# Optimization experiments

Measured on AMD Instinct MI355X. Metric: run time of the kernel, lower is better.

The kernel has to match this reference:

```python
import jax, jax.numpy as jnp
import numpy as np

DIM = 2048
N_HEADS = 16
HEAD_DIM = DIM // N_HEADS
ROPE_BASE = 10000.0


def rope_cos_sin(T, head_dim, dtype=jnp.float32):
    inv_freq = 1.0 / (ROPE_BASE ** (jnp.arange(0, head_dim, 2, dtype=jnp.float32) / head_dim))
    t = jnp.arange(T, dtype=jnp.float32)
    freqs = jnp.einsum('i,j->ij', t, inv_freq)          # [T, Hd/2]
    emb = jnp.concatenate([freqs, freqs], axis=-1)       # [T, Hd]
    return jnp.cos(emb).astype(dtype), jnp.sin(emb).astype(dtype)


def apply_rope(x, cos, sin):
    # x: [B,H,T,Hd]; cos/sin: [T,Hd]
    x1 = x[..., ::2]
    x2 = x[..., 1::2]
    # interleave (-x2, x1) back to [B,H,T,Hd]
    x_rot = jnp.stack([-x2, x1], axis=-1).reshape(x.shape)
    return x * cos[None, None, :, :] + x_rot * sin[None, None, :, :]


def setup_inputs() -> dict:
    key = jax.random.key(0)
    k1, k2, k3 = jax.random.split(key, 3)
    B, T = 2, 4096
    x = jax.random.normal(k1, (B, T, DIM), dtype=jnp.float32)
    w_qkv = jax.random.normal(k2, (3 * DIM, DIM), dtype=jnp.float32) * (1.0 / np.sqrt(DIM))
    w_proj = jax.random.normal(k3, (DIM, DIM), dtype=jnp.float32) * (1.0 / np.sqrt(DIM))
    return {"x": x, "w_qkv": w_qkv, "w_proj": w_proj}


def reference(x, w_qkv, w_proj):
    B, T, C = x.shape
    qkv = jnp.einsum('btc,dc->btd', x, w_qkv)            # [B,T,3C]
    q, k, v = jnp.split(qkv, 3, axis=-1)

    def split_heads(t):
        return t.reshape(B, T, N_HEADS, HEAD_DIM).transpose(0, 2, 1, 3)  # [B,H,T,Hd]

    q, k, v = split_heads(q), split_heads(k), split_heads(v)
    cos, sin = rope_cos_sin(T, HEAD_DIM, x.dtype)
    q = apply_rope(q, cos, sin)
    k = apply_rope(k, cos, sin)

    scale = 1.0 / np.sqrt(HEAD_DIM).astype(np.float32)
    att = jnp.einsum('bhqd,bhkd->bhqk', q, k) * scale     # [B,H,T,T]
    causal = jnp.tril(jnp.ones((T, T), dtype=bool))
    att = jnp.where(causal[None, None, :, :], att, jnp.finfo(att.dtype).min)
    att = jax.nn.softmax(att, axis=-1)
    out = jnp.einsum('bhqk,bhkd->bhqd', att, v)           # [B,H,T,Hd]
    out = out.transpose(0, 2, 1, 3).reshape(B, T, C)
    return jnp.einsum('btc,dc->btd', out, w_proj)
```

## Files before the change

kernel.cpp:

```cpp
#include <hip/hip_runtime.h>
#include <cstdint>
#include <cstddef>

#define B_SZ   2
#define T_SEQ  4096
#define DIM_   2048
#define NH_    16
#define HD_    128
#define QKVD   (3*DIM_)
#define SCALE_ 0.08838834764831845f

typedef __bf16 bf16x4 __attribute__((ext_vector_type(4)));
typedef __bf16 bf16x8 __attribute__((ext_vector_type(8)));
typedef float  f32x4  __attribute__((ext_vector_type(4)));

typedef const __attribute__((address_space(1))) void* gas_ptr_t;
typedef       __attribute__((address_space(3))) void* las_ptr_t;

#define GLOAD_LDS16(gp, lp) \
  __builtin_amdgcn_global_load_lds((gas_ptr_t)(gp), (las_ptr_t)(lp), 16, 0, 0)

__global__ void cast_f32_bf16(const float* __restrict__ in,
                              __bf16* __restrict__ out, int n4) {
  int i = blockIdx.x * blockDim.x + threadIdx.x;
  if (i < n4) {
    float4 v = ((const float4*)in)[i];
    bf16x4 o = { (__bf16)v.x, (__bf16)v.y, (__bf16)v.z, (__bf16)v.w };
    ((bf16x4*)out)[i] = o;
  }
}

__device__ __forceinline__ void store_c(float* C, size_t idx, float v)  { C[idx] = v; }
__device__ __forceinline__ void store_c(__bf16* C, size_t idx, float v) { C[idx] = (__bf16)v; }

template <typename OutT>
__global__ __launch_bounds__(256, 2) void gemm_bt(const __bf16* __restrict__ A,
                                                  const __bf16* __restrict__ B,
                                                  OutT* __restrict__ C,
                                                  int M, int N, int K) {
  __shared__ __attribute__((aligned(16))) __bf16 As[128 * 32];
  __shared__ __attribute__((aligned(16))) __bf16 Bs[128 * 32];

  const int tid  = threadIdx.x;
  const int wave = tid >> 6;
  const int lane = tid & 63;
  const int lrow = lane & 15;
  const int quad = lane >> 4;
  const int m0 = blockIdx.x * 128;
  const int n0 = blockIdx.y * 128;
  const int wm = (wave & 1) * 64;
  const int wn = (wave >> 1) * 64;

  const __bf16* Ag = A + (size_t)(m0 + (tid >> 2)) * K + (tid & 3) * 8;
  const __bf16* Bg = B + (size_t)(n0 + (tid >> 2)) * K + (tid & 3) * 8;

  f32x4 acc[4][4] = {};

  for (int k0 = 0; k0 < K; k0 += 32) {
    __syncthreads();
    GLOAD_LDS16(Ag + k0,                 &As[wave * 16 * 32]);
    GLOAD_LDS16(Ag + k0 + (size_t)64*K,  &As[(64 + wave * 16) * 32]);
    GLOAD_LDS16(Bg + k0,                 &Bs[wave * 16 * 32]);
    GLOAD_LDS16(Bg + k0 + (size_t)64*K,  &Bs[(64 + wave * 16) * 32]);
    __syncthreads();

    bf16x8 a[4], b[4];
#pragma unroll
    for (int i = 0; i < 4; i++)
      a[i] = *(const bf16x8*)&As[(wm + i * 16 + lrow) * 32 + quad * 8];
#pragma unroll
    for (int j = 0; j < 4; j++)
      b[j] = *(const bf16x8*)&Bs[(wn + j * 16 + lrow) * 32 + quad * 8];
#pragma unroll
    for (int i = 0; i < 4; i++)
#pragma unroll
      for (int j = 0; j < 4; j++)
        acc[i][j] = __builtin_amdgcn_mfma_f32_16x16x32_bf16(a[i], b[j], acc[i][j], 0, 0, 0);
  }

#pragma unroll
  for (int i = 0; i < 4; i++)
#pragma unroll
    for (int j = 0; j < 4; j++)
#pragma unroll
      for (int r = 0; r < 4; r++) {
        size_t row = (size_t)(m0 + wm + i * 16 + quad * 4 + r);
        size_t col = (size_t)(n0 + wn + j * 16 + lrow);
        store_c(C, row * (size_t)N + col, acc[i][j][r]);
      }
}

__global__ void rope_split(const __bf16* __restrict__ qkv,
                           __bf16* __restrict__ Qo,
                           __bf16* __restrict__ Ko,
                           __bf16* __restrict__ Vt) {
  const long id  = (long)blockIdx.x * blockDim.x + threadIdx.x;
  const int row = (int)(id / 3072);
  const int p   = (int)(id % 3072);
  const int b = row >> 12;
  const int t = row & (T_SEQ - 1);
  const __bf16* src = qkv + (size_t)row * QKVD;

  if (p < 2048) {
    const bool isq = (p < 1024);
    const int pp = isq ? p : p - 1024;
    const int dp = pp * 2;
    const int h = dp >> 7, d = dp & 127;
    const int base = isq ? 0 : DIM_;
    const float x0 = (float)src[base + dp];
    const float x1 = (float)src[base + dp + 1];
    const int i0 = d & 63, i1 = (d + 1) & 63;
    const float kf = -0.20762050593049014f;
    float a0 = (float)t * exp2f(i0 * kf);
    float a1 = (float)t * exp2f(i1 * kf);
    float s0, c0, s1, c1;
    sincosf(a0, &s0, &c0);
    sincosf(a1, &s1, &c1);
    float y0 = x0 * c0 - x1 * s0;
    float y1 = x1 * c1 + x0 * s1;
    __bf16* dst = (isq ? Qo : Ko) + (((size_t)(b * NH_ + h) * T_SEQ + t) * HD_ + d);
    dst[0] = (__bf16)y0;
    dst[1] = (__bf16)y1;
  } else {
    const int dp = (p - 2048) * 2;
    const int h = dp >> 7, d = dp & 127;
    __bf16 v0 = src[2 * DIM_ + dp];
    __bf16 v1 = src[2 * DIM_ + dp + 1];
    size_t base = (size_t)(b * NH_ + h) * HD_;
    Vt[(base + d)     * T_SEQ + t] = v0;
    Vt[(base + d + 1) * T_SEQ + t] = v1;
  }
}

__global__ __launch_bounds__(256, 2) void flash_attn(const __bf16* __restrict__ Q,
                                                     const __bf16* __restrict__ K,
                                                     const __bf16* __restrict__ Vt,
                                                     __bf16* __restrict__ O) {
  __shared__ __attribute__((aligned(16))) __bf16 Ks[64 * 136];
  __shared__ __attribute__((aligned(16))) __bf16 Vs[128 * 72];
  __shared__ __attribute__((aligned(16))) __bf16 Ps[4][32 * 72];

  const int qb   = (gridDim.x - 1) - blockIdx.x;
  const int bh   = blockIdx.y;
  const int tid  = threadIdx.x;
  const int wave = tid >> 6;
  const int lane = tid & 63;
  const int lrow = lane & 15;
  const int quad = lane >> 4;

  const __bf16* Qh = Q  + (size_t)bh * T_SEQ * HD_;
  const __bf16* Kh = K  + (size_t)bh * T_SEQ * HD_;
  const __bf16* Vh = Vt + (size_t)bh * HD_ * T_SEQ;

  const int q0 = qb * 128;
  const int qw = q0 + wave * 32;
  const int kcnt = 2 * qb + 2;

  bf16x8 qf[2][4];
#pragma unroll
  for (int qt = 0; qt < 2; qt++)
#pragma unroll
    for (int c = 0; c < 4; c++)
      qf[qt][c] = *(const bf16x8*)&Qh[(size_t)(qw + qt * 16 + lrow) * HD_ + c * 32 + quad * 8];

  f32x4 o[2][8] = {};
  float m_[2] = {-1e30f, -1e30f};
  float l_[2] = {0.f, 0.f};

  const int krow = tid >> 4, kch = tid & 15;
  const int vrow = tid >> 3, vch = tid & 7;

  bf16x8 kpre[4], vpre[4];
#pragma unroll
  for (int i = 0; i < 4; i++) {
    kpre[i] = *(const bf16x8*)&Kh[(size_t)(i * 16 + krow) * HD_ + kch * 8];
    vpre[i] = *(const bf16x8*)&Vh[(size_t)(i * 32 + vrow) * T_SEQ + vch * 8];
  }

  for (int kb = 0; kb < kcnt; ++kb) {
    __syncthreads();
#pragma unroll
    for (int i = 0; i < 4; i++) {
      *(bf16x8*)&Ks[(i * 16 + krow) * 136 + kch * 8] = kpre[i];
      *(bf16x8*)&Vs[(i * 32 + vrow) * 72  + vch * 8] = vpre[i];
    }
    __syncthreads();

    if (kb + 1 < kcnt) {
      const int nb = (kb + 1) * 64;
#pragma unroll
      for (int i = 0; i < 4; i++) {
        kpre[i] = *(const bf16x8*)&Kh[(size_t)(nb + i * 16 + krow) * HD_ + kch * 8];
        vpre[i] = *(const bf16x8*)&Vh[(size_t)(i * 32 + vrow) * T_SEQ + nb + vch * 8];
      }
    }

    const bool need_mask = (kb * 64 + 63) > qw;
    bool act[2];

#pragma unroll
    for (int qt = 0; qt < 2; qt++) {
      const int qbase = qw + qt * 16;
      act[qt] = (kb * 64) <= (qbase + 15);
      if (!act[qt]) continue;

      f32x4 st[4];
#pragma unroll
      for (int nt = 0; nt < 4; nt++) {
        f32x4 acc = {};
#pragma unroll
        for (int c = 0; c < 4; c++) {
          bf16x8 kf = *(const bf16x8*)&Ks[(nt * 16 + lrow) * 136 + c * 32 + quad * 8];
          acc = __builtin_amdgcn_mfma_f32_16x16x32_bf16(kf, qf[qt][c], acc, 0, 0, 0);
        }
        st[nt] = acc;
      }

      const int qglob = qbase + lrow;
      if (need_mask) {
#pragma unroll
        for (int nt = 0; nt < 4; nt++)
#pragma unroll
          for (int r = 0; r < 4; r++) {
            int key = kb * 64 + nt * 16 + quad * 4 + r;
            if (key > qglob) st[nt][r] = -1e30f;
          }
      }

      float mt = -1e30f;
#pragma unroll
      for (int nt = 0; nt < 4; nt++)
#pragma unroll
        for (int r = 0; r < 4; r++) mt = fmaxf(mt, st[nt][r]);
      mt = fmaxf(mt, __shfl_xor(mt, 16));
      mt = fmaxf(mt, __shfl_xor(mt, 32));
      const float mnew  = fmaxf(m_[qt], mt);
      const float alpha = __expf((m_[qt] - mnew) * SCALE_);
      m_[qt] = mnew;

      float psum = 0.f;
#pragma unroll
      for (int nt = 0; nt < 4; nt++) {
        bf16x4 pk;
#pragma unroll
        for (int r = 0; r < 4; r++) {
          float pv = __expf((st[nt][r] - mnew) * SCALE_);
          psum += pv;
          pk[r] = (__bf16)pv;
        }
        *(bf16x4*)&Ps[wave][(qt * 16 + lrow) * 72 + nt * 16 + quad * 4] = pk;
      }
      psum += __shfl_xor(psum, 16);
      psum += __shfl_xor(psum, 32);
      l_[qt] = l_[qt] * alpha + psum;

      float ab[4];
#pragma unroll
      for (int r = 0; r < 4; r++) ab[r] = __shfl(alpha, quad * 4 + r);
#pragma unroll
      for (int dt = 0; dt < 8; dt++)
#pragma unroll
        for (int r = 0; r < 4; r++) o[qt][dt][r] *= ab[r];
    }

    __asm__ volatile("s_waitcnt lgkmcnt(0)" ::: "memory");

#pragma unroll
    for (int qt = 0; qt < 2; qt++) {
      if (!act[qt]) continue;
      bf16x8 pf[2];
#pragma unroll
      for (int c2 = 0; c2 < 2; c2++)
        pf[c2] = *(const bf16x8*)&Ps[wave][(qt * 16 + lrow) * 72 + c2 * 32 + quad * 8];
#pragma unroll
      for (int dt = 0; dt < 8; dt++)
#pragma unroll
        for (int c2 = 0; c2 < 2; c2++) {
          bf16x8 vf = *(const bf16x8*)&Vs[(dt * 16 + lrow) * 72 + c2 * 32 + quad * 8];
          o[qt][dt] = __builtin_amdgcn_mfma_f32_16x16x32_bf16(pf[c2], vf, o[qt][dt], 0, 0, 0);
        }
    }
  }

  const int b = bh >> 4, h = bh & 15;
#pragma unroll
  for (int qt = 0; qt < 2; qt++) {
    float linv[4];
#pragma unroll
    for (int r = 0; r < 4; r++) linv[r] = 1.f / __shfl(l_[qt], quad * 4 + r);
#pragma unroll
    for (int dt = 0; dt < 8; dt++)
#pragma unroll
      for (int r = 0; r < 4; r++) {
        int t = qw + qt * 16 + quad * 4 + r;
        size_t idx = (((size_t)b * T_SEQ + t) * NH_ + h) * HD_ + dt * 16 + lrow;
        O[idx] = (__bf16)(o[qt][dt][r] * linv[r]);
      }
  }
}

extern "C" void kernel_launch(void* const* d_in, const int* in_sizes, int n_in,
                              void* d_out, int out_size, void* d_ws, size_t ws_size,
                              hipStream_t stream) {
  const float* x      = (const float*)d_in[0];
  const float* w_qkv  = (const float*)d_in[1];
  const float* w_proj = (const float*)d_in[2];
  float* out = (float*)d_out;

  char* ws = (char*)d_ws;
  const size_t SZ_X16   = (size_t)B_SZ * T_SEQ * DIM_ * 2;
  const size_t SZ_W16   = (size_t)QKVD * DIM_ * 2;
  const size_t SZ_WP16  = (size_t)DIM_ * DIM_ * 2;
  const size_t SZ_QKV16 = (size_t)B_SZ * T_SEQ * QKVD * 2;
  const size_t SZ_HEADS = SZ_X16;

  __bf16* x16   = (__bf16*)(ws);
  __bf16* w16   = (__bf16*)(ws + SZ_X16);
  __bf16* wp16  = (__bf16*)(ws + SZ_X16 + SZ_W16);
  __bf16* qkv16 = (__bf16*)(ws + SZ_X16 + SZ_W16 + SZ_WP16);
  __bf16* K16   = (__bf16*)(ws + SZ_X16 + SZ_W16 + SZ_WP16 + SZ_QKV16);
  __bf16* Vt16  = (__bf16*)(ws + SZ_X16 + SZ_W16 + SZ_WP16 + SZ_QKV16 + SZ_HEADS);
  __bf16* Q16   = x16;
  __bf16* O16   = qkv16;

  const size_t NEED = SZ_X16 + SZ_W16 + SZ_WP16 + SZ_QKV16 + 2 * SZ_HEADS;
  if (ws_size < NEED) return;

  {
    int n4 = (int)((size_t)B_SZ * T_SEQ * DIM_ / 4);
    cast_f32_bf16<<<(n4 + 255) / 256, 256, 0, stream>>>(x, x16, n4);
    n4 = (int)((size_t)QKVD * DIM_ / 4);
    cast_f32_bf16<<<(n4 + 255) / 256, 256, 0, stream>>>(w_qkv, w16, n4);
    n4 = (int)((size_t)DIM_ * DIM_ / 4);
    cast_f32_bf16<<<(n4 + 255) / 256, 256, 0, stream>>>(w_proj, wp16, n4);
  }

  gemm_bt<__bf16><<<dim3(8192 / 128, QKVD / 128), 256, 0, stream>>>(
      x16, w16, qkv16, 8192, QKVD, DIM_);

  {
    long total = (long)B_SZ * T_SEQ * 3072;
    rope_split<<<(int)(total / 256), 256, 0, stream>>>(qkv16, Q16, K16, Vt16);
  }

  flash_attn<<<dim3(T_SEQ / 128, B_SZ * NH_), 256, 0, stream>>>(Q16, K16, Vt16, O16);

  gemm_bt<float><<<dim3(8192 / 128, DIM_ / 128), 256, 0, stream>>>(
      O16, wp16, out, 8192, DIM_, DIM_);
}
```

Measured before the change: 998.1 us.

## Double-buffer K/V tiles in LDS with XOR swizzle and fused q-tile MFMA

The flash attention kernel now keeps two LDS buffers for K and V. Each iteration stores the next tile from registers into the spare buffer and issues global loads two tiles ahead, so only one barrier per iteration remains. Row padding is replaced by an XOR swizzle on the 16-byte chunks of K, V and P to avoid LDS bank conflicts with denser storage. The two query sub-tiles now share each K and V fragment load across paired MFMAs, at the cost of doubled LDS usage and more live registers.

```diff
diff --git a/kernel.cpp b/kernel.cpp
--- a/kernel.cpp
+++ b/kernel.cpp
@@ -136,166 +136,180 @@
                                                      const __bf16* __restrict__ K,
                                                      const __bf16* __restrict__ Vt,
                                                      __bf16* __restrict__ O) {
-  __shared__ __attribute__((aligned(16))) __bf16 Ks[64 * 136];
-  __shared__ __attribute__((aligned(16))) __bf16 Vs[128 * 72];
-  __shared__ __attribute__((aligned(16))) __bf16 Ps[4][32 * 72];
+  __shared__ __attribute__((aligned(16))) __bf16 Ks[2][64 * 128];
+  __shared__ __attribute__((aligned(16))) __bf16 Vs[2][128 * 64];
+  __shared__ __attribute__((aligned(16))) __bf16 Ps[4][32 * 64];
 
   const int qb   = (gridDim.x - 1) - blockIdx.x;
   const int bh   = blockIdx.y;
   const int tid  = threadIdx.x;
   const int wave = tid >> 6;
   const int lane = tid & 63;
-  const int lrow = lane & 15;
+  const int l15  = lane & 15;
   const int quad = lane >> 4;
 
   const __bf16* Qh = Q  + (size_t)bh * T_SEQ * HD_;
   const __bf16* Kh = K  + (size_t)bh * T_SEQ * HD_;
   const __bf16* Vh = Vt + (size_t)bh * HD_ * T_SEQ;
 
-  const int q0 = qb * 128;
-  const int qw = q0 + wave * 32;
+  const int qw   = qb * 128 + wave * 32;
   const int kcnt = 2 * qb + 2;
 
   bf16x8 qf[2][4];
 #pragma unroll
   for (int qt = 0; qt < 2; qt++)
 #pragma unroll
-    for (int c = 0; c < 4; c++)
-      qf[qt][c] = *(const bf16x8*)&Qh[(size_t)(qw + qt * 16 + lrow) * HD_ + c * 32 + quad * 8];
+    for (int kc = 0; kc < 4; kc++)
+      qf[qt][kc] = *(const bf16x8*)&Qh[(size_t)(qw + qt * 16 + l15) * HD_ + kc * 32 + quad * 8];
 
   f32x4 o[2][8] = {};
   float m_[2] = {-1e30f, -1e30f};
   float l_[2] = {0.f, 0.f};
 
-  const int krow = tid >> 4, kch = tid & 15;
-  const int vrow = tid >> 3, vch = tid & 7;
+  const int krow = tid >> 2, kq4 = tid & 3;
+  const int vrow = tid >> 1, vh2 = tid & 1;
 
   bf16x8 kpre[4], vpre[4];
-#pragma unroll
-  for (int i = 0; i < 4; i++) {
-    kpre[i] = *(const bf16x8*)&Kh[(size_t)(i * 16 + krow) * HD_ + kch * 8];
-    vpre[i] = *(const bf16x8*)&Vh[(size_t)(i * 32 + vrow) * T_SEQ + vch * 8];
-  }
+
+#define LOAD_TILES(KB)                                                          \
+  {                                                                             \
+    const __bf16* kg = Kh + (size_t)((KB) * 64 + krow) * HD_;                   \
+    const __bf16* vg = Vh + (size_t)vrow * T_SEQ + (KB) * 64;                   \
+    _Pragma("unroll")                                                           \
+    for (int j = 0; j < 4; j++) {                                               \
+      kpre[j] = *(const bf16x8*)&kg[(j * 4 + kq4) * 8];                         \
+      vpre[j] = *(const bf16x8*)&vg[(vh2 * 4 + j) * 8];                         \
+    }                                                                           \
+  }
+
+#define STORE_TILES(BUF)                                                        \
+  {                                                                             \
+    _Pragma("unroll")                                                           \
+    for (int j = 0; j < 4; j++) {                                               \
+      int kc_ = (j * 4 + kq4) ^ (krow & 7);                                     \
+      *(bf16x8*)&Ks[BUF][krow * 128 + kc_ * 8] = kpre[j];                       \
+      int vc_ = (vh2 * 4 + j) ^ (vrow & 7);                                     \
+      *(bf16x8*)&Vs[BUF][vrow * 64 + vc_ * 8] = vpre[j];                        \
+    }                                                                           \
+  }
+
+  LOAD_TILES(0);
+  STORE_TILES(0);
+  if (kcnt > 1) LOAD_TILES(1);
+  __syncthreads();
 
   for (int kb = 0; kb < kcnt; ++kb) {
-    __syncthreads();
-#pragma unroll
-    for (int i = 0; i < 4; i++) {
-      *(bf16x8*)&Ks[(i * 16 + krow) * 136 + kch * 8] = kpre[i];
-      *(bf16x8*)&Vs[(i * 32 + vrow) * 72  + vch * 8] = vpre[i];
+    const int cur = kb & 1;
+    if (kb + 1 < kcnt) STORE_TILES((kb + 1) & 1);
+    if (kb + 2 < kcnt) LOAD_TILES(kb + 2);
+
+    if (kb * 64 <= qw + 31) {
+      f32x4 st[2][4];
+#pragma unroll
+      for (int kt = 0; kt < 4; kt++) {
+        f32x4 a0 = {}, a1 = {};
+        const int row = kt * 16 + l15;
+#pragma unroll
+        for (int kc = 0; kc < 4; kc++) {
+          const int c = kc * 4 + quad;
+          bf16x8 kf = *(const bf16x8*)&Ks[cur][row * 128 + (c ^ (row & 7)) * 8];
+          a0 = __builtin_amdgcn_mfma_f32_16x16x32_bf16(kf, qf[0][kc], a0, 0, 0, 0);
+          a1 = __builtin_amdgcn_mfma_f32_16x16x32_bf16(kf, qf[1][kc], a1, 0, 0, 0);
+        }
+        st[0][kt] = a0; st[1][kt] = a1;
+      }
+
+      if (kb * 64 + 63 > qw) {
+#pragma unroll
+        for (int qt = 0; qt < 2; qt++)
+#pragma unroll
+          for (int kt = 0; kt < 4; kt++)
+#pragma unroll
+            for (int r = 0; r < 4; r++) {
+              int key = kb * 64 + kt * 16 + quad * 4 + r;
+              int q   = qw + qt * 16 + l15;
+              if (key > q) st[qt][kt][r] = -1e30f;
+            }
+      }
+
+      float alpha[2];
+#pragma unroll
+      for (int qt = 0; qt < 2; qt++) {
+        float mt = -1e30f;
+#pragma unroll
+        for (int kt = 0; kt < 4; kt++)
+#pragma unroll
+          for (int r = 0; r < 4; r++) mt = fmaxf(mt, st[qt][kt][r]);
+        mt = fmaxf(mt, __shfl_xor(mt, 16));
+        mt = fmaxf(mt, __shfl_xor(mt, 32));
+        const float mnew = fmaxf(m_[qt], mt);
+        alpha[qt] = __expf((m_[qt] - mnew) * SCALE_);
+        m_[qt] = mnew;
+
+        float ps = 0.f;
+        const int prow = qt * 16 + l15;
+#pragma unroll
+        for (int kt = 0; kt < 4; kt++) {
+          bf16x4 pk;
+#pragma unroll
+          for (int r = 0; r < 4; r++) {
+            float pv = __expf((st[qt][kt][r] - mnew) * SCALE_);
+            ps += pv;
+            pk[r] = (__bf16)pv;
+          }
+          const int ec = kt * 16 + quad * 4;
+          const int c  = (ec >> 3) ^ (prow & 7);
+          *(bf16x4*)&Ps[wave][prow * 64 + c * 8 + (ec & 7)] = pk;
+        }
+        ps += __shfl_xor(ps, 16);
+        ps += __shfl_xor(ps, 32);
+        l_[qt] = l_[qt] * alpha[qt] + ps;
+      }
+
+      __asm__ volatile("s_waitcnt lgkmcnt(0)" ::: "memory");
+
+#pragma unroll
+      for (int qt = 0; qt < 2; qt++)
+#pragma unroll
+        for (int r = 0; r < 4; r++) {
+          float a = __shfl(alpha[qt], quad * 4 + r);
+#pragma unroll
+          for (int dt = 0; dt < 8; dt++) o[qt][dt][r] *= a;
+        }
+
+#pragma unroll
+      for (int kc2 = 0; kc2 < 2; kc2++) {
+        const int ec = kc2 * 32 + quad * 8;
+        const int pc = (ec >> 3) ^ (l15 & 7);
+        bf16x8 pf0 = *(const bf16x8*)&Ps[wave][(l15)      * 64 + pc * 8];
+        bf16x8 pf1 = *(const bf16x8*)&Ps[wave][(16 + l15) * 64 + pc * 8];
+#pragma unroll
+        for (int dt = 0; dt < 8; dt++) {
+          const int vr = dt * 16 + l15;
+          const int vc = (ec >> 3) ^ (vr & 7);
+          bf16x8 vf = *(const bf16x8*)&Vs[cur][vr * 64 + vc * 8];
+          o[0][dt] = __builtin_amdgcn_mfma_f32_16x16x32_bf16(pf0, vf, o[0][dt], 0, 0, 0);
+          o[1][dt] = __builtin_amdgcn_mfma_f32_16x16x32_bf16(pf1, vf, o[1][dt], 0, 0, 0);
+        }
+      }
     }
     __syncthreads();
-
-    if (kb + 1 < kcnt) {
-      const int nb = (kb + 1) * 64;
-#pragma unroll
-      for (int i = 0; i < 4; i++) {
-        kpre[i] = *(const bf16x8*)&Kh[(size_t)(nb + i * 16 + krow) * HD_ + kch * 8];
-        vpre[i] = *(const bf16x8*)&Vh[(size_t)(i * 32 + vrow) * T_SEQ + nb + vch * 8];
+  }
+
+  const int b = bh >> 4, h = bh & 15;
+#pragma unroll
+  for (int qt = 0; qt < 2; qt++) {
+    float il = 1.f / l_[qt];
+#pragma unroll
+    for (int r = 0; r < 4; r++) {
+      float linv = __shfl(il, quad * 4 + r);
+      int t = qw + qt * 16 + quad * 4 + r;
+#pragma unroll
+      for (int dt = 0; dt < 8; dt++) {
+        size_t idx = (((size_t)b * T_SEQ + t) * NH_ + h) * HD_ + dt * 16 + l15;
+        O[idx] = (__bf16)(o[qt][dt][r] * linv);
       }
     }
-
-    const bool need_mask = (kb * 64 + 63) > qw;
-    bool act[2];
-
-#pragma unroll
-    for (int qt = 0; qt < 2; qt++) {
-      const int qbase = qw + qt * 16;
-      act[qt] = (kb * 64) <= (qbase + 15);
-      if (!act[qt]) continue;
-
-      f32x4 st[4];
-#pragma unroll
-      for (int nt = 0; nt < 4; nt++) {
-        f32x4 acc = {};
-#pragma unroll
-        for (int c = 0; c < 4; c++) {
-          bf16x8 kf = *(const bf16x8*)&Ks[(nt * 16 + lrow) * 136 + c * 32 + quad * 8];
-          acc = __builtin_amdgcn_mfma_f32_16x16x32_bf16(kf, qf[qt][c], acc, 0, 0, 0);
-        }
-        st[nt] = acc;
-      }
-
-      const int qglob = qbase + lrow;
-      if (need_mask) {
-#pragma unroll
-        for (int nt = 0; nt < 4; nt++)
-#pragma unroll
-          for (int r = 0; r < 4; r++) {
-            int key = kb * 64 + nt * 16 + quad * 4 + r;
-            if (key > qglob) st[nt][r] = -1e30f;
-          }
-      }
-
-      float mt = -1e30f;
-#pragma unroll
-      for (int nt = 0; nt < 4; nt++)
-#pragma unroll
-        for (int r = 0; r < 4; r++) mt = fmaxf(mt, st[nt][r]);
-      mt = fmaxf(mt, __shfl_xor(mt, 16));
-      mt = fmaxf(mt, __shfl_xor(mt, 32));
-      const float mnew  = fmaxf(m_[qt], mt);
-      const float alpha = __expf((m_[qt] - mnew) * SCALE_);
-      m_[qt] = mnew;
-
-      float psum = 0.f;
-#pragma unroll
-      for (int nt = 0; nt < 4; nt++) {
-        bf16x4 pk;
-#pragma unroll
-        for (int r = 0; r < 4; r++) {
-          float pv = __expf((st[nt][r] - mnew) * SCALE_);
-          psum += pv;
-          pk[r] = (__bf16)pv;
-        }
-        *(bf16x4*)&Ps[wave][(qt * 16 + lrow) * 72 + nt * 16 + quad * 4] = pk;
-      }
-      psum += __shfl_xor(psum, 16);
-      psum += __shfl_xor(psum, 32);
-      l_[qt] = l_[qt] * alpha + psum;
-
-      float ab[4];
-#pragma unroll
-      for (int r = 0; r < 4; r++) ab[r] = __shfl(alpha, quad * 4 + r);
-#pragma unroll
-      for (int dt = 0; dt < 8; dt++)
-#pragma unroll
-        for (int r = 0; r < 4; r++) o[qt][dt][r] *= ab[r];
-    }
-
-    __asm__ volatile("s_waitcnt lgkmcnt(0)" ::: "memory");
-
-#pragma unroll
-    for (int qt = 0; qt < 2; qt++) {
-      if (!act[qt]) continue;
-      bf16x8 pf[2];
-#pragma unroll
-      for (int c2 = 0; c2 < 2; c2++)
-        pf[c2] = *(const bf16x8*)&Ps[wave][(qt * 16 + lrow) * 72 + c2 * 32 + quad * 8];
-#pragma unroll
-      for (int dt = 0; dt < 8; dt++)
-#pragma unroll
-        for (int c2 = 0; c2 < 2; c2++) {
-          bf16x8 vf = *(const bf16x8*)&Vs[(dt * 16 + lrow) * 72 + c2 * 32 + quad * 8];
-          o[qt][dt] = __builtin_amdgcn_mfma_f32_16x16x32_bf16(pf[c2], vf, o[qt][dt], 0, 0, 0);
-        }
-    }
-  }
-
-  const int b = bh >> 4, h = bh & 15;
-#pragma unroll
-  for (int qt = 0; qt < 2; qt++) {
-    float linv[4];
-#pragma unroll
-    for (int r = 0; r < 4; r++) linv[r] = 1.f / __shfl(l_[qt], quad * 4 + r);
-#pragma unroll
-    for (int dt = 0; dt < 8; dt++)
-#pragma unroll
-      for (int r = 0; r < 4; r++) {
-        int t = qw + qt * 16 + quad * 4 + r;
-        size_t idx = (((size_t)b * T_SEQ + t) * NH_ + h) * HD_ + dt * 16 + lrow;
-        O[idx] = (__bf16)(o[qt][dt][r] * linv[r]);
-      }
   }
 }
 
```

New measurement: 928.8 us. 1.07x faster.
